# Kernel tuning notes

Measured on AMD Instinct MI355X. Metric: run time of the kernel, lower is better.

The kernel has to match this reference:

```python
import jax, jax.numpy as jnp
import numpy as np

B, L, D = 4, 2048, 1024
H, DH = 16, 64
W = 128            # window_len
CS, R = 32, 1      # chunk_size, chunk_rank
CACHE = 2048
NCC = CACHE // CS * R   # compressed cache vectors (64)
NCB = L // CS * R       # compressed block vectors (64)
NC = NCC + NCB          # total compressed vectors (128)
NQ = L // CS            # query chunks (64)
T = L // W              # query tiles (16)
NEG = jnp.float32(-1e30)


def _ln(x, g, b, eps=1e-5):
    m = x.mean(-1, keepdims=True)
    v = ((x - m) ** 2).mean(-1, keepdims=True)
    return (x - m) * jax.lax.rsqrt(v + eps) * g + b


def _scores(x, Wd, bd):
    # dconv_1 + per-chunk softmax over chunk_size positions
    b = x.shape[0]; nc = x.shape[1] // CS
    s = (x @ Wd + bd).reshape(b, nc, CS, H, R)
    s = jnp.transpose(s, (0, 3, 1, 4, 2))          # b,H,nc,R,CS
    return jax.nn.softmax(s.astype(jnp.float32), axis=-1).astype(x.dtype)


def _compress(x, sc):
    b = x.shape[0]; nc = x.shape[1] // CS
    xv = jnp.transpose(x.reshape(b, nc, CS, H, DH), (0, 3, 1, 2, 4))  # b,H,nc,CS,DH
    return (sc @ xv).reshape(b, H, nc * R, DH)


def _heads(x):
    b, l, _ = x.shape
    return jnp.transpose(x.reshape(b, l, H, DH), (0, 2, 1, 3))


def _rel_shift(x):
    # Transformer-XL style relative shift, chunk variant (zeros enter from padding)
    b = x.shape[0]; nc = x.shape[-1]
    x5 = jnp.transpose(x.reshape(b, H, NQ, CS, nc), (0, 1, 3, 2, 4))  # b,H,CS,NQ,nc
    xp = jnp.pad(x5, ((0, 0), (0, 0), (0, 0), (0, 0), (0, R))).reshape(b, H, CS, NQ * (nc + R))
    idx = NQ * R + jnp.arange(NQ)[:, None] * nc + jnp.arange(nc)[None, :]
    out = jnp.take(xp, idx.reshape(-1), axis=-1).reshape(b, H, CS, NQ, nc)
    return jnp.transpose(out, (0, 1, 3, 2, 4)).reshape(b, H, L, nc)


def _forward(h, h_cache, key_pe, pos_win, Wq, Wk, Wv, Wo, Wd, bd, Wr, br, Wrc, brc,
             r_r_bias, r_w_bias, g_dproj, b_dproj, g_win, b_win, mask):
    b = h.shape[0]
    q = _heads(h @ Wq) / np.float32(np.sqrt(DH))       # b,H,L,DH (pre-scaled)

    # --- compressed cache keys/values ---
    hcc = _compress(h_cache, _scores(h_cache, Wd, bd))           # b,H,NCC,DH
    hcm = jnp.transpose(hcc, (0, 2, 1, 3)).reshape(b, -1, D)
    k_cache = _heads(_ln(hcm @ Wk, g_dproj, b_dproj))
    v_cache = _heads(_ln(hcm @ Wv, g_dproj, b_dproj))

    # --- sliding window keys/values (last W of cache + current block) ---
    k_bp = h @ Wk
    v_bp = h @ Wv
    hw = h_cache[:, -W:]
    k_win = _ln(jnp.concatenate([hw @ Wk, k_bp], 1), g_win, b_win)   # b, W+L, D
    v_win = _ln(jnp.concatenate([hw @ Wv, v_bp], 1), g_win, b_win)

    # --- compressed current-block keys/values ---
    sc = _scores(h, Wd, bd)
    k_bpc = _heads(_ln(jnp.transpose(_compress(k_bp, sc), (0, 2, 1, 3)).reshape(b, -1, D), g_dproj, b_dproj))
    v_bpc = _heads(_ln(jnp.transpose(_compress(v_bp, sc), (0, 2, 1, 3)).reshape(b, -1, D), g_dproj, b_dproj))
    k_comp = jnp.concatenate([k_cache, k_bpc], 2)     # b,H,NC,DH
    v_comp = jnp.concatenate([v_cache, v_bpc], 2)

    # --- windowed attention (tiled, as_strided equivalent via gather) ---
    ti = jnp.arange(T)[:, None] * W + jnp.arange(2 * W)[None, :]     # (T, 2W)
    k_t = jnp.transpose(k_win[:, ti].reshape(b, T, 2 * W, H, DH), (0, 3, 1, 2, 4))  # b,H,T,2W,DH
    v_t = jnp.transpose(v_win[:, ti].reshape(b, T, 2 * W, H, DH), (0, 3, 1, 2, 4))
    q_t = q.reshape(b, H, T, W, DH)
    aw = jnp.einsum('bhtqd,bhtkd->bhtqk', q_t + r_w_bias, k_t)       # b,H,T,W,2W
    # diagonal extraction: row q keeps cols q+1 .. q+W (the W causal window keys)
    dcol = jnp.arange(W)[:, None] + 1 + jnp.arange(W)[None, :]       # (W, W)
    aw = jnp.take_along_axis(aw, dcol[None, None, None], axis=-1).reshape(b, H, L, W)
    pos_t = (pos_win @ Wr + br).reshape(W, H, DH)
    aw = aw + jnp.einsum('bhld,whd->bhlw', q + r_r_bias, pos_t)

    # --- compressed (chunk) attention ---
    ac = jnp.einsum('bhld,bhcd->bhlc', q, k_comp)
    pos_c = (key_pe @ Wrc + brc).reshape(NC, H, DH)
    ac = ac + _rel_shift(jnp.einsum('bhld,chd->bhlc', q, pos_c))
    ac = jnp.where(mask, NEG, ac.reshape(b, H, NQ, CS, NC)).reshape(b, H, L, NC)

    # --- joint softmax over [compressed | window] ---
    full = jax.nn.softmax(jnp.concatenate([ac, aw], -1).astype(jnp.float32), -1).astype(h.dtype)
    ac, aw = full[..., :NC], full[..., NC:]

    # --- put_tiles: scatter window probs back to tiled 2W layout (inverse of diag extract) ---
    awt = aw.reshape(b, H, T, W, W)
    awp = jnp.pad(awt, ((0, 0), (0, 0), (0, 0), (0, 0), (1, W)))     # last dim 1+2W, zeros outside band
    col = jnp.clip(jnp.arange(2 * W)[None, :] - jnp.arange(W)[:, None], 0, 2 * W)
    aw_t = jnp.take_along_axis(awp, col[None, None, None], axis=-1)  # b,H,T,W,2W

    out = jnp.einsum('bhlc,bhcd->bhld', ac, v_comp) + \
          jnp.einsum('bhtqk,bhtkd->bhtqd', aw_t, v_t).reshape(b, H, L, DH)
    out = jnp.transpose(out, (0, 2, 1, 3)).reshape(b, L, D)
    return out @ Wo


def setup_inputs() -> dict:
    key = jax.random.key(0)
    ks = jax.random.split(key, 16)
    p = lambda i, shape: jax.random.normal(ks[i], shape, jnp.float32) * 0.02
    inp = dict(
        h=jax.random.normal(ks[0], (B, L, D), jnp.float32),
        h_cache=jax.random.normal(ks[1], (B, CACHE, D), jnp.float32),
        key_pe=jax.random.normal(ks[2], (NC, D), jnp.float32),
        pos_embed_window=jax.random.normal(ks[3], (W, D), jnp.float32),
        Wq=p(4, (D, D)), Wk=p(5, (D, D)), Wv=p(6, (D, D)), Wo=p(7, (D, D)),
        Wd=p(8, (D, H * R)), bd=jnp.zeros((H * R,), jnp.float32),
        Wr=p(9, (D, D)), br=jnp.zeros((D,), jnp.float32),
        Wrc=p(10, (D, D)), brc=jnp.zeros((D,), jnp.float32),
        r_r_bias=p(11, (1, H, 1, DH)), r_w_bias=p(12, (1, H, 1, 1, DH)),
        g_dproj=jnp.ones((D,), jnp.float32), b_dproj=jnp.zeros((D,), jnp.float32),
        g_win=jnp.ones((D,), jnp.float32), b_win=jnp.zeros((D,), jnp.float32),
    )
    # causal mask over compressed vectors: bp chunk c visible to query chunk j only if c < j
    jq = jnp.arange(NQ)[:, None]
    cc = jnp.arange(NCB // R)[None, :]
    mbp = jnp.repeat(cc >= jq, R, axis=1)                         # (NQ, NCB)
    mask = jnp.concatenate([jnp.zeros((NQ, NCC), bool), mbp], axis=1)
    inp['chunked_attn_mask'] = mask[None, None, :, None, :]       # (1,1,NQ,1,NC)
    return inp


def reference(h, h_cache, key_pe, pos_embed_window, Wq, Wk, Wv, Wo, Wd, bd, Wr, br,
              Wrc, brc, r_r_bias, r_w_bias, g_dproj, b_dproj, g_win, b_win,
              chunked_attn_mask):
    return _forward(h, h_cache, key_pe, pos_embed_window, Wq, Wk, Wv, Wo, Wd, bd,
                    Wr, br, Wrc, brc, r_r_bias, r_w_bias, g_dproj, b_dproj,
                    g_win, b_win, chunked_attn_mask)
```

## Files before the change

### kernel.cpp

```cpp
#include <hip/hip_runtime.h>


typedef unsigned short u16;
typedef __attribute__((ext_vector_type(8))) short short8;
typedef __attribute__((ext_vector_type(4))) float f32x4;

#define NEGINF -1e30f

__device__ __forceinline__ float bf2f(u16 u) {
    union { unsigned int i; float f; } v; v.i = ((unsigned int)u) << 16; return v.f;
}
__device__ __forceinline__ u16 f2bf(float f) {
    union { float fl; unsigned int i; } v; v.fl = f;
    unsigned int x = v.i;
    return (u16)((x + 0x7fffu + ((x >> 16) & 1u)) >> 16);
}
__device__ __forceinline__ short8 ldg8(const u16* p) { return *(const short8*)p; }

__device__ __forceinline__ void async16(const u16* g, u16* l) {
    __builtin_amdgcn_global_load_lds(
        (const __attribute__((address_space(1))) unsigned int*)g,
        (__attribute__((address_space(3))) unsigned int*)l, 16, 0, 0);
}

__global__ __launch_bounds__(256) void cast_f2b(const float* __restrict__ s,
                                                u16* __restrict__ d, int n4)
{
    int i = blockIdx.x * 256 + threadIdx.x;
    if (i >= n4) return;
    float4 v = ((const float4*)s)[i];
    u16* o = d + i * 4;
    o[0] = f2bf(v.x); o[1] = f2bf(v.y); o[2] = f2bf(v.z); o[3] = f2bf(v.w);
}

__global__ __launch_bounds__(256) void cast_win(const float* __restrict__ hc,
                                                u16* __restrict__ d)
{
    int i = blockIdx.x * 256 + threadIdx.x;
    int flat = i * 4;
    int b = flat >> 17, r = (flat >> 10) & 127, c = flat & 1023;
    float4 v = *(const float4*)(hc + ((long)b * 2048 + 1920 + r) * 1024 + c);
    u16* o = d + (long)flat;
    o[0] = f2bf(v.x); o[1] = f2bf(v.y); o[2] = f2bf(v.z); o[3] = f2bf(v.w);
}

__global__ __launch_bounds__(256) void cast_transpose6(
    const float* __restrict__ W0, const float* __restrict__ W1,
    const float* __restrict__ W2, const float* __restrict__ W3,
    const float* __restrict__ W4, const float* __restrict__ W5,
    u16* __restrict__ D0, u16* __restrict__ D1, u16* __restrict__ D2,
    u16* __restrict__ D3, u16* __restrict__ D4, u16* __restrict__ D5)
{
    const int z = blockIdx.z;
    const float* W = (z == 0) ? W0 : (z == 1) ? W1 : (z == 2) ? W2
                   : (z == 3) ? W3 : (z == 4) ? W4 : W5;
    u16* WT = (z == 0) ? D0 : (z == 1) ? D1 : (z == 2) ? D2
            : (z == 3) ? D3 : (z == 4) ? D4 : D5;

    __shared__ float t[32][33];
    const int bx = blockIdx.x, by = blockIdx.y;
    const int tx = threadIdx.x & 31, ty = threadIdx.x >> 5;
    #pragma unroll
    for (int p = 0; p < 4; ++p) {
        int k = by * 32 + ty + p * 8;
        t[ty + p * 8][tx] = W[(long)k * 1024 + bx * 32 + tx];
    }
    __syncthreads();
    #pragma unroll
    for (int p = 0; p < 4; ++p) {
        int n = ty + p * 8;
        WT[((long)(bx * 32 + n)) * 1024 + by * 32 + tx] = f2bf(t[tx][n]);
    }
}

__global__ __launch_bounds__(256) void cast_wd(const float* __restrict__ Wd,
                                               u16* __restrict__ WdB)
{
    int e = blockIdx.x * 256 + threadIdx.x;
    if (e < 16384) {
        int n = e & 15, k = e >> 4;
        WdB[n * 1024 + k] = f2bf(Wd[e]);
    }
}

#define GEMM_P3_BODY(EPILOGUE)                                                  \
    const int tid = threadIdx.x;                                                \
    const int bm = blockIdx.x, bn = blockIdx.y;                                 \
    const int K = 1024, NT = 32;                                                \
    __shared__ __align__(16) u16 As[3 * 128 * 32];                              \
    __shared__ __align__(16) u16 Bs[3 * 128 * 32];                              \
    const int lane = tid & 63, wv = tid >> 6;                                   \
    const int l15 = lane & 15, quad = lane >> 4;                                \
    const int wm = (wv & 1) * 64, wn = (wv >> 1) * 64;                          \
    f32x4 acc[4][4];                                                            \
    _Pragma("unroll")                                                           \
    for (int i = 0; i < 4; ++i)                                                 \
        _Pragma("unroll")                                                       \
        for (int j = 0; j < 4; ++j) acc[i][j] = (f32x4){0.f, 0.f, 0.f, 0.f};    \
    const int srow = wv * 32 + (lane >> 2);                                     \
    const int scol = (lane & 3) * 8;                                            \
    const u16* a_src  = A  + (long)(bm * 128 + srow) * K + scol;                \
    const u16* a_src2 = a_src + (long)16 * K;                                   \
    const u16* b_src  = Bt + (long)(bn * 128 + srow) * K + scol;                \
    const u16* b_src2 = b_src + (long)16 * K;                                   \
    const int lofs0 = (wv * 32) * 32;                                           \
    const int lofs1 = (wv * 32 + 16) * 32;                                      \
    auto stage = [&](int t, int cur) {                                          \
        const int k0 = t * 32;                                                  \
        async16(a_src  + k0, &As[cur * 4096 + lofs0]);                          \
        async16(a_src2 + k0, &As[cur * 4096 + lofs1]);                          \
        async16(b_src  + k0, &Bs[cur * 4096 + lofs0]);                          \
        async16(b_src2 + k0, &Bs[cur * 4096 + lofs1]);                          \
    };                                                                          \
    stage(0, 0); stage(1, 1);                                                   \
    int cur = 0;                                                                \
    for (int t = 0; t < NT; ++t) {                                              \
        if (t == NT - 1)                                                        \
            asm volatile("s_waitcnt vmcnt(0) lgkmcnt(0)\ns_barrier" ::: "memory"); \
        else                                                                    \
            asm volatile("s_waitcnt vmcnt(4) lgkmcnt(0)\ns_barrier" ::: "memory"); \
        int nxt = cur + 2; if (nxt >= 3) nxt -= 3;                              \
        if (t + 2 < NT) stage(t + 2, nxt);                                      \
        const u16* as = &As[cur * 4096];                                        \
        const u16* bs = &Bs[cur * 4096];                                        \
        short8 af[4], bfr[4];                                                   \
        _Pragma("unroll")                                                       \
        for (int i = 0; i < 4; ++i)                                             \
            af[i] = *(const short8*)&as[(wm + i * 16 + l15) * 32 + quad * 8];   \
        _Pragma("unroll")                                                       \
        for (int j = 0; j < 4; ++j)                                             \
            bfr[j] = *(const short8*)&bs[(wn + j * 16 + l15) * 32 + quad * 8];  \
        _Pragma("unroll")                                                       \
        for (int i = 0; i < 4; ++i)                                             \
            _Pragma("unroll")                                                   \
            for (int j = 0; j < 4; ++j)                                         \
                acc[i][j] = __builtin_amdgcn_mfma_f32_16x16x32_bf16(af[i], bfr[j], acc[i][j], 0, 0, 0); \
        cur = (cur + 1 == 3) ? 0 : cur + 1;                                     \
    }                                                                           \
    EPILOGUE

__global__ __launch_bounds__(256) void gemm_qkv3(
    const u16* __restrict__ A, const u16* __restrict__ Bt,
    u16* __restrict__ q_ws, float* __restrict__ kbp, float* __restrict__ vbp)
{
    GEMM_P3_BODY({
        const int mat = bn >> 3;
        _Pragma("unroll")
        for (int i = 0; i < 4; ++i) {
            _Pragma("unroll")
            for (int j = 0; j < 4; ++j) {
                int col = (bn & 7) * 128 + wn + j * 16 + l15;
                _Pragma("unroll")
                for (int r = 0; r < 4; ++r) {
                    int row = bm * 128 + wm + i * 16 + quad * 4 + r;
                    float v = acc[i][j][r];
                    long idx = (long)row * 1024 + col;
                    if (mat == 0)      q_ws[idx] = f2bf(v * 0.125f);
                    else if (mat == 1) kbp[idx] = v;
                    else               vbp[idx] = v;
                }
            }
        }
    })
}

__global__ __launch_bounds__(256) void gemm_out3(
    const u16* __restrict__ A, const u16* __restrict__ Bt,
    float* __restrict__ Cf)
{
    GEMM_P3_BODY({
        _Pragma("unroll")
        for (int i = 0; i < 4; ++i) {
            _Pragma("unroll")
            for (int j = 0; j < 4; ++j) {
                int col = bn * 128 + wn + j * 16 + l15;
                _Pragma("unroll")
                for (int r = 0; r < 4; ++r) {
                    int row = bm * 128 + wm + i * 16 + quad * 4 + r;
                    Cf[(long)row * 1024 + col] = acc[i][j][r];
                }
            }
        }
    })
}

struct GJob {
    const u16* A; long ab;
    const u16* Bt;
    float* Cf; u16* Cb; long cb;
    const float* bias; float scale;
};

// ... 54 lines not shown
        for (int jx = 0; jx < 4; ++jx) {
            int col = bn * 128 + wn + jx * 16 + l15;
            float bsv = j.bias ? j.bias[col] : 0.f;
            #pragma unroll
            for (int r = 0; r < 4; ++r) {
                int row = bm * 128 + wm + i * 16 + quad * 4 + r;
                float v = acc[i][jx][r] * j.scale + bsv;
                long idx = coff + (long)row * N + col;
                if (j.Cf) j.Cf[idx] = v;
                if (j.Cb) j.Cb[idx] = f2bf(v);
            }
        }
    }
}

__global__ __launch_bounds__(256) void gemm_dual(GJob j0, GJob j1, int nz0, int N, int K)
{
    const bool first = ((int)blockIdx.z < nz0);
    const int bz = first ? blockIdx.z : blockIdx.z - nz0;
    if (first) gemm_core128(j0, bz, blockIdx.x, blockIdx.y, N, K);
    else       gemm_core128(j1, bz, blockIdx.x, blockIdx.y, N, K);
}

__global__ __launch_bounds__(256) void gemm_multi4(GJob j0, GJob j1, GJob j2, GJob j3,
                                                   int n0, int n1, int n2, int N, int K)
{
    const int z = blockIdx.z;
    if (z < n0)                gemm_core128(j0, z, blockIdx.x, blockIdx.y, N, K);
    else if (z < n0 + n1)      gemm_core128(j1, z - n0, blockIdx.x, blockIdx.y, N, K);
    else if (z < n0 + n1 + n2) gemm_core128(j2, z - n0 - n1, blockIdx.x, blockIdx.y, N, K);
    else                       gemm_core128(j3, z - n0 - n1 - n2, blockIdx.x, blockIdx.y, N, K);
}

__global__ __launch_bounds__(256) void scores_compress(
    const float* __restrict__ srcF, const u16* __restrict__ srcB, long src_bstride,
    const u16* __restrict__ WdB, const float* __restrict__ bd,
    u16* __restrict__ out_comp, long comp_bstride,
    float* __restrict__ out_sc, long sc_bstride)
{
    const int c = blockIdx.x, b = blockIdx.y;
    const int tid = threadIdx.x;
    const int lane = tid & 63, wv = tid >> 6;
    const int l15 = lane & 15, quad = lane >> 4;

    __shared__ __align__(16) u16 srcs[32][1032];
    __shared__ float sred[4][32][16];
    __shared__ float s_sm[32][16];

    if (srcB) {
        const u16* sb = srcB + (long)b * src_bstride + (long)c * 32 * 1024;
        for (int e = tid; e < 4096; e += 256) {
            int flat = e * 8;
            int row = flat >> 10, col = flat & 1023;
            *(short8*)&srcs[row][col] = ldg8(sb + (long)row * 1024 + col);
        }
    } else {
        const float* sb = srcF + (long)b * src_bstride + (long)c * 32 * 1024;
        for (int e = tid; e < 8192; e += 256) {
            int flat = e * 4;
            int row = flat >> 10, col = flat & 1023;
            float4 v = *(const float4*)(sb + (long)row * 1024 + col);
            u16* dp = &srcs[row][col];
            dp[0] = f2bf(v.x); dp[1] = f2bf(v.y); dp[2] = f2bf(v.z); dp[3] = f2bf(v.w);
        }
    }
    __syncthreads();

    {
        f32x4 acc0 = {0.f,0.f,0.f,0.f}, acc1 = {0.f,0.f,0.f,0.f};
        const int kq = wv * 256;
        #pragma unroll
        for (int kc = 0; kc < 8; ++kc) {
            int off = kq + kc * 32 + quad * 8;
            short8 bf_ = ldg8(WdB + (long)l15 * 1024 + off);
            short8 a0 = *(const short8*)&srcs[l15][off];
            short8 a1 = *(const short8*)&srcs[16 + l15][off];
            acc0 = __builtin_amdgcn_mfma_f32_16x16x32_bf16(a0, bf_, acc0, 0, 0, 0);
            acc1 = __builtin_amdgcn_mfma_f32_16x16x32_bf16(a1, bf_, acc1, 0, 0, 0);
        }
        #pragma unroll
        for (int r = 0; r < 4; ++r) {
            sred[wv][quad * 4 + r][l15]      = acc0[r];
            sred[wv][16 + quad * 4 + r][l15] = acc1[r];
        }
    }
    __syncthreads();
    for (int idx = tid; idx < 512; idx += 256) {
        int i = idx >> 4, hd = idx & 15;
        s_sm[i][hd] = bd[hd] + sred[0][i][hd] + sred[1][i][hd]
                            + sred[2][i][hd] + sred[3][i][hd];
    }
    __syncthreads();

    if (tid < 16) {
        int hd = tid;
        float m = NEGINF;
        for (int i = 0; i < 32; ++i) m = fmaxf(m, s_sm[i][hd]);
        float s = 0.f;
        for (int i = 0; i < 32; ++i) s += __expf(s_sm[i][hd] - m);
        float inv = 1.f / s;
        for (int i = 0; i < 32; ++i) s_sm[i][hd] = __expf(s_sm[i][hd] - m) * inv;
    }
    __syncthreads();

    if (out_sc) {
        for (int idx = tid; idx < 512; idx += 256) {
            int hd = idx >> 5, i = idx & 31;
            out_sc[(long)b * sc_bstride + ((long)hd * 64 + c) * 32 + i] = s_sm[i][hd];
        }
    }
    if (out_comp) {
        #pragma unroll
        for (int p = 0; p < 4; ++p) {
            int j = tid + p * 256;
            int hd = j >> 6;
            float acc = 0.f;
            for (int i = 0; i < 32; ++i) acc += s_sm[i][hd] * bf2f(srcs[i][j]);
            out_comp[(long)b * comp_bstride + (long)c * 1024 + j] = f2bf(acc);
        }
    }
}

__global__ __launch_bounds__(256) void compress_kv_ln(
    const float* __restrict__ kbp, const float* __restrict__ vbp,
    const float* __restrict__ sc,
    const float* __restrict__ g, const float* __restrict__ be,
    u16* __restrict__ k_comp, u16* __restrict__ vcT)
{
    const int c = blockIdx.x, b = blockIdx.y;
    const int tid = threadIdx.x;
    const int lane = tid & 63, wv = tid >> 6;

    __shared__ float scw[16][32];
    __shared__ float red[4][4];

    for (int idx = tid; idx < 512; idx += 256) {
        int hd = idx >> 5, i = idx & 31;
        scw[hd][i] = sc[((long)(b * 16 + hd) * 64 + c) * 32 + i];
    }
    __syncthreads();

    float xk[4], xv[4];
    #pragma unroll
    for (int p = 0; p < 4; ++p) {
        int j = tid + p * 256;
        int hd = j >> 6;
        float ak = 0.f, av = 0.f;
        for (int i = 0; i < 32; ++i) {
            float w = scw[hd][i];
            long off = ((long)b * 2048 + c * 32 + i) * 1024 + j;
            ak += w * kbp[off];
            av += w * vbp[off];
        }
        xk[p] = ak; xv[p] = av;
    }
    float sk = 0.f, qk = 0.f, sv = 0.f, qv = 0.f;
    #pragma unroll
    for (int p = 0; p < 4; ++p) { sk += xk[p]; qk += xk[p]*xk[p]; sv += xv[p]; qv += xv[p]*xv[p]; }
    for (int off = 32; off; off >>= 1) {
        sk += __shfl_xor(sk, off); qk += __shfl_xor(qk, off);
        sv += __shfl_xor(sv, off); qv += __shfl_xor(qv, off);
    }
    if (lane == 0) { red[0][wv] = sk; red[1][wv] = qk; red[2][wv] = sv; red[3][wv] = qv; }
    __syncthreads();
    sk = red[0][0] + red[0][1] + red[0][2] + red[0][3];
    qk = red[1][0] + red[1][1] + red[1][2] + red[1][3];
    sv = red[2][0] + red[2][1] + red[2][2] + red[2][3];
    qv = red[3][0] + red[3][1] + red[3][2] + red[3][3];
    const float inv_n = 1.f / 1024.f;
    float mk = sk * inv_n, mv = sv * inv_n;
    float ik = rsqrtf(fmaxf(qk * inv_n - mk * mk, 0.f) + 1e-5f);
    float iv = rsqrtf(fmaxf(qv * inv_n - mv * mv, 0.f) + 1e-5f);
    #pragma unroll
    for (int p = 0; p < 4; ++p) {
        int j = tid + p * 256;
        k_comp[((long)b * 128 + 64 + c) * 1024 + j] = f2bf((xk[p] - mk) * ik * g[j] + be[j]);
        vcT[((long)b * 1024 + j) * 128 + 64 + c]   = f2bf((xv[p] - mv) * iv * g[j] + be[j]);
    }
}

__global__ __launch_bounds__(256) void ln_rows_kv(
    const float* __restrict__ kc, const float* __restrict__ vc,
    const float* __restrict__ g, const float* __restrict__ be,
    u16* __restrict__ k_comp, u16* __restrict__ vcT)
{
    const int gr = blockIdx.x;
    const int b = gr >> 6, r = gr & 63;
    const float* pk = kc + ((long)b * 64 + r) * 1024;
    const float* pv = vc + ((long)b * 64 + r) * 1024;
    const int tid = threadIdx.x;
    const int lane = tid & 63, wv = tid >> 6;

    __shared__ float red[4][4];
    float xk[4], xv[4];
    float smk = 0.f, sqk = 0.f, smv = 0.f, sqv = 0.f;
    #pragma unroll
    for (int p = 0; p < 4; ++p) {
        xk[p] = pk[tid + p * 256];
        xv[p] = pv[tid + p * 256];
        smk += xk[p]; sqk += xk[p] * xk[p];
        smv += xv[p]; sqv += xv[p] * xv[p];
    }
    for (int off = 32; off; off >>= 1) {
        smk += __shfl_xor(smk, off); sqk += __shfl_xor(sqk, off);
        smv += __shfl_xor(smv, off); sqv += __shfl_xor(sqv, off);
    }
    if (lane == 0) { red[0][wv] = smk; red[1][wv] = sqk; red[2][wv] = smv; red[3][wv] = sqv; }
    __syncthreads();
    smk = red[0][0] + red[0][1] + red[0][2] + red[0][3];
    sqk = red[1][0] + red[1][1] + red[1][2] + red[1][3];
    smv = red[2][0] + red[2][1] + red[2][2] + red[2][3];
    sqv = red[3][0] + red[3][1] + red[3][2] + red[3][3];
    const float inv_n = 1.f / 1024.f;
    float mk = smk * inv_n, mv = smv * inv_n;
    float ik = rsqrtf(fmaxf(sqk * inv_n - mk * mk, 0.f) + 1e-5f);
    float iv = rsqrtf(fmaxf(sqv * inv_n - mv * mv, 0.f) + 1e-5f);
    #pragma unroll
    for (int p = 0; p < 4; ++p) {
        int j = tid + p * 256;
        k_comp[((long)b * 128 + r) * 1024 + j] = f2bf((xk[p] - mk) * ik * g[j] + be[j]);
        vcT[((long)b * 1024 + j) * 128 + r]    = f2bf((xv[p] - mv) * iv * g[j] + be[j]);
    }
}

__global__ __launch_bounds__(256) void row_stats2(
    const float* __restrict__ s1, const float* __restrict__ s2, long src_bstride,
    float2* __restrict__ d1, float2* __restrict__ d2, long dst_bstride,
    long dst_row_off, int rows_per_batch)
{
    const int gr = blockIdx.x;
    const int b = gr / rows_per_batch, r = gr % rows_per_batch;
    const float* p1 = s1 + (long)b * src_bstride + (long)r * 1024;
    const float* p2 = s2 + (long)b * src_bstride + (long)r * 1024;
    const int tid = threadIdx.x;
    const int lane = tid & 63, wv = tid >> 6;

    __shared__ float red[4][4];
    float sm1 = 0.f, sq1 = 0.f, sm2 = 0.f, sq2 = 0.f;
    #pragma unroll
    for (int p = 0; p < 4; ++p) {
        float x = p1[tid + p * 256];
        float y = p2[tid + p * 256];
        sm1 += x; sq1 += x * x;
        sm2 += y; sq2 += y * y;
    }
    for (int off = 32; off; off >>= 1) {
        sm1 += __shfl_xor(sm1, off); sq1 += __shfl_xor(sq1, off);
        sm2 += __shfl_xor(sm2, off); sq2 += __shfl_xor(sq2, off);
    }
    if (lane == 0) { red[0][wv] = sm1; red[1][wv] = sq1; red[2][wv] = sm2; red[3][wv] = sq2; }
    __syncthreads();
    if (tid == 0) {
        sm1 = red[0][0] + red[0][1] + red[0][2] + red[0][3];
        sq1 = red[1][0] + red[1][1] + red[1][2] + red[1][3];
        sm2 = red[2][0] + red[2][1] + red[2][2] + red[2][3];
        sq2 = red[3][0] + red[3][1] + red[3][2] + red[3][3];
        float m1 = sm1 * (1.f / 1024.f);
        float i1 = rsqrtf(fmaxf(sq1 * (1.f / 1024.f) - m1 * m1, 0.f) + 1e-5f);
        float m2 = sm2 * (1.f / 1024.f);
        float i2 = rsqrtf(fmaxf(sq2 * (1.f / 1024.f) - m2 * m2, 0.f) + 1e-5f);
        d1[(long)b * dst_bstride + dst_row_off + r] = make_float2(m1, i1);
        d2[(long)b * dst_bstride + dst_row_off + r] = make_float2(m2, i2);
    }
}

__global__ __launch_bounds__(256) void win_apply(
    const float* __restrict__ kcw, const float* __restrict__ vcw,
    const float* __restrict__ kbp, const float* __restrict__ vbp,
    const float2* __restrict__ st_kw, const float2* __restrict__ st_vw,
    const float* __restrict__ g_w, const float* __restrict__ b_w,
    u16* __restrict__ kwin, u16* __restrict__ vwinT)
{
    const int tt = blockIdx.x, dc = blockIdx.y, b = blockIdx.z;
    const int t0 = tt * 64, d0 = dc * 64;
    const int tid = threadIdx.x;

    __shared__ u16 vt[64][74];

    const int r = tid >> 2;
    const int dsub = (tid & 3) * 16;
    const int t = t0 + r;
    const float* ks; const float* vs;
    if (t < 128) {
        ks = kcw + ((long)b * 128 + t) * 1024;
        vs = vcw + ((long)b * 128 + t) * 1024;
    } else {
        ks = kbp + ((long)b * 2048 + t - 128) * 1024;
        vs = vbp + ((long)b * 2048 + t - 128) * 1024;
    }
    float2 sk = st_kw[(long)b * 2176 + t];
    float2 sv = st_vw[(long)b * 2176 + t];
    #pragma unroll
    for (int j = 0; j < 16; j += 4) {
        int d = d0 + dsub + j;
        float4 kv = *(const float4*)(ks + d);
        float4 vv = *(const float4*)(vs + d);
        float4 g4 = *(const float4*)(g_w + d);
        float4 b4 = *(const float4*)(b_w + d);
        u16 ko[4];
        ko[0] = f2bf((kv.x - sk.x) * sk.y * g4.x + b4.x);
        ko[1] = f2bf((kv.y - sk.x) * sk.y * g4.y + b4.y);
        ko[2] = f2bf((kv.z - sk.x) * sk.y * g4.z + b4.z);
        ko[3] = f2bf((kv.w - sk.x) * sk.y * g4.w + b4.w);
        *(uint2*)&kwin[((long)b * 2176 + t) * 1024 + d] = *(const uint2*)ko;
        vt[r][dsub + j + 0] = f2bf((vv.x - sv.x) * sv.y * g4.x + b4.x);
        vt[r][dsub + j + 1] = f2bf((vv.y - sv.x) * sv.y * g4.y + b4.y);
        vt[r][dsub + j + 2] = f2bf((vv.z - sv.x) * sv.y * g4.z + b4.z);
        vt[r][dsub + j + 3] = f2bf((vv.w - sv.x) * sv.y * g4.w + b4.w);
    }
    __syncthreads();
    #pragma unroll
    for (int pass = 0; pass < 16; ++pass) {
        int dd = (tid >> 6) + pass * 4;
        int rr = tid & 63;
        int crow = t0 + rr;
        if (crow >= 1)
            vwinT[((long)b * 1024 + d0 + dd) * 2176 + crow - 1] = vt[rr][dd];
    }
}

__global__ __launch_bounds__(256, 4) void attention(
    const u16* __restrict__ qb,
    const u16* __restrict__ kcb,
    const u16* __restrict__ vcT,
    const u16* __restrict__ kwb,
    const u16* __restrict__ vwT,
    const u16* __restrict__ pcb,
    const u16* __restrict__ ptb,
    const float* __restrict__ r_w,
// ... 103 lines not shown
                for (int j = 0; j < 8; ++j) f[j] = (short)f2bf(bf2f((u16)qv[j]) + bb[j]);
                qf[kc][hf] = f;
            }
        }
        for (int nt = wv; nt < 10; nt += 4) {
            int t = nt * 16 + l15;
            int row = l0 + 1 + t; if (row > 2175) row = 2175;
            f32x4 a0 = {0.f,0.f,0.f,0.f}, a1 = {0.f,0.f,0.f,0.f};
            #pragma unroll
            for (int kc = 0; kc < 2; ++kc) {
                int k0 = kc * 32;
                short8 bk = ldg8(kwb + ((long)(b * 2176 + row)) * 1024 + h * 64 + k0 + quad * 8);
                a0 = __builtin_amdgcn_mfma_f32_16x16x32_bf16(qf[kc][0], bk, a0, 0, 0, 0);
                a1 = __builtin_amdgcn_mfma_f32_16x16x32_bf16(qf[kc][1], bk, a1, 0, 0, 0);
            }
            s1a[nw] = a0; s1b[nw] = a1; nts[nw] = nt; ++nw;
        }
    }
    __builtin_amdgcn_s_setprio(0);
    __syncthreads();
    for (int i = 0; i < nw; ++i) {
        int t = nts[i] * 16 + l15;
        #pragma unroll
        for (int r = 0; r < 4; ++r) {
            int r0 = quad * 4 + r;
            int w0 = t - r0;
            if (w0 >= 0 && w0 < 128) L[r0 * 260 + 128 + w0] += s1a[i][r];
            int r1 = 16 + quad * 4 + r;
            int w1 = t - r1;
            if (w1 >= 0 && w1 < 128) L[r1 * 260 + 128 + w1] += s1b[i][r];
        }
    }
    __syncthreads();

    #pragma unroll
    for (int rr = 0; rr < 8; ++rr) {
        const int r = wv * 8 + rr;
        float4 v = *(const float4*)&L[r * 260 + lane * 4];
        float m = fmaxf(fmaxf(v.x, v.y), fmaxf(v.z, v.w));
        for (int off = 32; off; off >>= 1) m = fmaxf(m, __shfl_xor(m, off));
        float e0 = __expf(v.x - m), e1 = __expf(v.y - m);
        float e2 = __expf(v.z - m), e3 = __expf(v.w - m);
        float s = (e0 + e1) + (e2 + e3);
        for (int off = 32; off; off >>= 1) s += __shfl_xor(s, off);
        float inv = 1.f / s;
        e0 *= inv; e1 *= inv; e2 *= inv; e3 *= inv;
        u16* rowP = Lu + (long)r * 520;
        if (lane < 32) {
            u16 pk[4] = {f2bf(e0), f2bf(e1), f2bf(e2), f2bf(e3)};
            *(uint2*)&rowP[lane * 4] = *(const uint2*)pk;
        } else {
            const int l = lane - 32;
            const int t = 4 * l + r;
            u16* p = rowP + 160 + t;
            p[0] = f2bf(e0); p[1] = f2bf(e1); p[2] = f2bf(e2); p[3] = f2bf(e3);
            const int tz = (l < r) ? l : 128 + l;
            rowP[160 + tz] = 0;
        }
    }
    __syncthreads();

    __builtin_amdgcn_s_setprio(1);
    const int n0d = wv * 16;
    f32x4 o0 = {0.f,0.f,0.f,0.f}, o1 = {0.f,0.f,0.f,0.f};
    #pragma unroll
    for (int kc = 0; kc < 4; ++kc) {
        int k0 = kc * 32;
        short8 bv = ldg8(vcT + ((long)(b * 1024 + h * 64 + n0d + l15)) * 128 + k0 + quad * 8);
        short8 av0 = *(const short8*)(Lu + (long)l15 * 520 + k0 + quad * 8);
        short8 av1 = *(const short8*)(Lu + (long)(16 + l15) * 520 + k0 + quad * 8);
        o0 = __builtin_amdgcn_mfma_f32_16x16x32_bf16(av0, bv, o0, 0, 0, 0);
        o1 = __builtin_amdgcn_mfma_f32_16x16x32_bf16(av1, bv, o1, 0, 0, 0);
    }
    #pragma unroll
    for (int kc = 0; kc < 5; ++kc) {
        int k0 = kc * 32;
        short8 bv = ldg8(vwT + ((long)(b * 1024 + h * 64 + n0d + l15)) * 2176 + l0 + k0 + quad * 8);
        short8 av0 = *(const short8*)(Lu + (long)l15 * 520 + 160 + k0 + quad * 8);
        short8 av1 = *(const short8*)(Lu + (long)(16 + l15) * 520 + 160 + k0 + quad * 8);
        o0 = __builtin_amdgcn_mfma_f32_16x16x32_bf16(av0, bv, o0, 0, 0, 0);
        o1 = __builtin_amdgcn_mfma_f32_16x16x32_bf16(av1, bv, o1, 0, 0, 0);
    }
    __builtin_amdgcn_s_setprio(0);
    #pragma unroll
    for (int r = 0; r < 4; ++r) {
        int r0 = quad * 4 + r, r1 = 16 + quad * 4 + r;
        attn_o[((long)(b * 2048 + l0 + r0)) * 1024 + h * 64 + n0d + l15] = f2bf(o0[r]);
        attn_o[((long)(b * 2048 + l0 + r1)) * 1024 + h * 64 + n0d + l15] = f2bf(o1[r]);
    }
}

extern "C" void kernel_launch(void* const* d_in, const int* in_sizes, int n_in,
                              void* d_out, int out_size, void* d_ws, size_t ws_size,
                              hipStream_t stream)
{
    (void)in_sizes; (void)n_in; (void)out_size; (void)ws_size;

    const float* h       = (const float*)d_in[0];
    const float* h_cache = (const float*)d_in[1];
    const float* key_pe  = (const float*)d_in[2];
    const float* pos_w   = (const float*)d_in[3];
    const float* Wq      = (const float*)d_in[4];
    const float* Wk      = (const float*)d_in[5];
    const float* Wv      = (const float*)d_in[6];
    const float* Wo      = (const float*)d_in[7];
    const float* Wd      = (const float*)d_in[8];
    const float* bd      = (const float*)d_in[9];
    const float* Wr      = (const float*)d_in[10];
    const float* br      = (const float*)d_in[11];
    const float* Wrc     = (const float*)d_in[12];
    const float* brc     = (const float*)d_in[13];
    const float* r_r     = (const float*)d_in[14];
    const float* r_w     = (const float*)d_in[15];
    const float* g_d     = (const float*)d_in[16];
    const float* b_d     = (const float*)d_in[17];
    const float* g_w     = (const float*)d_in[18];
    const float* b_w     = (const float*)d_in[19];

    char* ws = (char*)d_ws;
    size_t off = 0;
    auto alloc = [&](size_t bytes) -> void* {
        void* p = ws + off; off += (bytes + 255) & ~(size_t)255; return p;
    };
    u16* hB     = (u16*)alloc((size_t)8192 * 1024 * 2);
    u16* hcwB   = (u16*)alloc((size_t)4 * 128 * 1024 * 2);
    u16* WqkvT  = (u16*)alloc((size_t)3 * 1024 * 1024 * 2);
    u16* WoT    = (u16*)alloc((size_t)1024 * 1024 * 2);
    u16* WrT    = (u16*)alloc((size_t)1024 * 1024 * 2);
    u16* WrcT   = (u16*)alloc((size_t)1024 * 1024 * 2);
    u16* pwB    = (u16*)alloc((size_t)128 * 1024 * 2);
    u16* kpeB   = (u16*)alloc((size_t)128 * 1024 * 2);
    u16* WdB    = (u16*)alloc((size_t)16 * 1024 * 2);
    u16*   q_ws   = (u16*)alloc((size_t)8192 * 1024 * 2);
    float* kbp    = (float*)alloc((size_t)8192 * 1024 * 4);
    float* vbp    = (float*)alloc((size_t)8192 * 1024 * 4);
    u16*   attn_o = (u16*)alloc((size_t)8192 * 1024 * 2);
    float* kcw    = (float*)alloc((size_t)4 * 128 * 1024 * 4);
    float* vcw    = (float*)alloc((size_t)4 * 128 * 1024 * 4);
    u16*   hcm    = (u16*)alloc((size_t)4 * 64 * 1024 * 2);
    float* kc_raw = (float*)alloc((size_t)4 * 64 * 1024 * 4);
    float* vc_raw = (float*)alloc((size_t)4 * 64 * 1024 * 4);
    float* sc_blk = (float*)alloc((size_t)4 * 16 * 64 * 32 * 4);
    u16*   k_comp = (u16*)alloc((size_t)4 * 128 * 1024 * 2);
    u16*   vcT    = (u16*)alloc((size_t)4 * 1024 * 128 * 2);
    float2* st_kw = (float2*)alloc((size_t)4 * 2176 * 8);
    float2* st_vw = (float2*)alloc((size_t)4 * 2176 * 8);
    u16*   pos_tb = (u16*)alloc((size_t)128 * 1024 * 2);
    u16*   pos_cb = (u16*)alloc((size_t)128 * 1024 * 2);
    u16*   kwin   = (u16*)alloc((size_t)4 * 2176 * 1024 * 2);
    u16*   vwinT  = (u16*)alloc((size_t)4 * 1024 * 2176 * 2 + 256);

    const u16* WkT = WqkvT + (size_t)1024 * 1024;
    const u16* WvT = WqkvT + (size_t)2 * 1024 * 1024;

    const dim3 blk(256);

    cast_f2b<<<dim3(8192), blk, 0, stream>>>(h, hB, 2097152);
    cast_win<<<dim3(512), blk, 0, stream>>>(h_cache, hcwB);
    cast_transpose6<<<dim3(32,32,6), blk, 0, stream>>>(
        Wq, Wk, Wv, Wo, Wr, Wrc,
        WqkvT, WqkvT + (size_t)1024*1024, WqkvT + (size_t)2*1024*1024,
        WoT, WrT, WrcT);
    cast_f2b<<<dim3(128), blk, 0, stream>>>(pos_w, pwB, 32768);
    cast_f2b<<<dim3(128), blk, 0, stream>>>(key_pe, kpeB, 32768);
    cast_wd<<<dim3(64), blk, 0, stream>>>(Wd, WdB);

    {
        GJob jk = { hcwB, (long)128*1024, WkT, kcw, nullptr, (long)128*1024, nullptr, 1.f };
        GJob jv = { hcwB, (long)128*1024, WvT, vcw, nullptr, (long)128*1024, nullptr, 1.f };
        GJob jt = { pwB,  0, WrT,  nullptr, pos_tb, 0, br,  1.f };
        GJob jc = { kpeB, 0, WrcT, nullptr, pos_cb, 0, brc, 1.f };
        gemm_multi4<<<dim3(1,8,10), blk, 0, stream>>>(jk, jv, jt, jc, 4, 4, 1, 1024, 1024);
    }

    gemm_qkv3<<<dim3(64,24,1), blk, 0, stream>>>(hB, WqkvT, q_ws, kbp, vbp);

    scores_compress<<<dim3(64,4), blk, 0, stream>>>(h_cache, nullptr, (long)2048*1024, WdB, bd,
                                                    hcm, (long)64*1024, nullptr, 0);
    scores_compress<<<dim3(64,4), blk, 0, stream>>>(nullptr, hB, (long)2048*1024, WdB, bd,
                                                    nullptr, 0, sc_blk, (long)16*64*32);

    {
        GJob jk = { hcm, 0, WkT, kc_raw, nullptr, 0, nullptr, 1.f };
        GJob jv = { hcm, 0, WvT, vc_raw, nullptr, 0, nullptr, 1.f };
        gemm_dual<<<dim3(2,8,2), blk, 0, stream>>>(jk, jv, 1, 1024, 1024);
    }

    compress_kv_ln<<<dim3(64,4), blk, 0, stream>>>(kbp, vbp, sc_blk, g_d, b_d, k_comp, vcT);
    ln_rows_kv<<<dim3(256), blk, 0, stream>>>(kc_raw, vc_raw, g_d, b_d, k_comp, vcT);

    row_stats2<<<dim3(512),  blk, 0, stream>>>(kcw, vcw, (long)128*1024,  st_kw, st_vw, 2176, 0,   128);
    row_stats2<<<dim3(8192), blk, 0, stream>>>(kbp, vbp, (long)2048*1024, st_kw, st_vw, 2176, 128, 2048);
    win_apply<<<dim3(34,16,4), blk, 0, stream>>>(kcw, vcw, kbp, vbp, st_kw, st_vw, g_w, b_w, kwin, vwinT);

    attention<<<dim3(64,16,4), blk, 0, stream>>>(q_ws, k_comp, vcT, kwin, vwinT,
                                                 pos_cb, pos_tb, r_w, r_r, attn_o);
    gemm_out3<<<dim3(64,8,1), blk, 0, stream>>>(attn_o, WoT, (float*)d_out);
}
```

Measured before the change: 513.9 us.

## Store block K/V projections in bf16, merge cast and stats launches, prefetch V

The block K/V projection outputs (kbp, vbp) are now written in bf16 instead of fp32, which halves their write and read traffic in the compress, row-stats and window-apply kernels. The small cast kernels, the two scores_compress launches and the two row_stats launches are each merged into a single launch to cut launch overhead. The attention kernel now loads its V fragments into registers before the softmax phase so the global loads overlap with it. The risks are rounding K/V to bf16 before the LayerNorm statistics and extra register pressure in attention.

Measured after the change: 508.5 us. About the same (-1.0%).

```diff
diff --git a/kernel.cpp b/kernel.cpp
--- a/kernel.cpp
+++ b/kernel.cpp
@@ -23,25 +23,40 @@
         (__attribute__((address_space(3))) unsigned int*)l, 16, 0, 0);
 }
 
-__global__ __launch_bounds__(256) void cast_f2b(const float* __restrict__ s,
-                                                u16* __restrict__ d, int n4)
-{
-    int i = blockIdx.x * 256 + threadIdx.x;
-    if (i >= n4) return;
-    float4 v = ((const float4*)s)[i];
-    u16* o = d + i * 4;
-    o[0] = f2bf(v.x); o[1] = f2bf(v.y); o[2] = f2bf(v.z); o[3] = f2bf(v.w);
-}
-
-__global__ __launch_bounds__(256) void cast_win(const float* __restrict__ hc,
-                                                u16* __restrict__ d)
-{
-    int i = blockIdx.x * 256 + threadIdx.x;
-    int flat = i * 4;
-    int b = flat >> 17, r = (flat >> 10) & 127, c = flat & 1023;
-    float4 v = *(const float4*)(hc + ((long)b * 2048 + 1920 + r) * 1024 + c);
-    u16* o = d + (long)flat;
-    o[0] = f2bf(v.x); o[1] = f2bf(v.y); o[2] = f2bf(v.z); o[3] = f2bf(v.w);
+__global__ __launch_bounds__(256) void cast_all(
+    const float* __restrict__ h, const float* __restrict__ hc,
+    const float* __restrict__ pos_w, const float* __restrict__ key_pe,
+    const float* __restrict__ Wd,
+    u16* __restrict__ hB, u16* __restrict__ hcwB,
+    u16* __restrict__ pwB, u16* __restrict__ kpeB, u16* __restrict__ WdB)
+{
+    const int bx = blockIdx.x, tid = threadIdx.x;
+    if (bx < 8192) {
+        int i = bx * 256 + tid;
+        float4 v = ((const float4*)h)[i];
+        u16* o = hB + (long)i * 4;
+        o[0] = f2bf(v.x); o[1] = f2bf(v.y); o[2] = f2bf(v.z); o[3] = f2bf(v.w);
+    } else if (bx < 8704) {
+        int i = (bx - 8192) * 256 + tid;
+        int flat = i * 4;
+        int b = flat >> 17, r = (flat >> 10) & 127, c = flat & 1023;
+        float4 v = *(const float4*)(hc + ((long)b * 2048 + 1920 + r) * 1024 + c);
+        u16* o = hcwB + (long)flat;
+        o[0] = f2bf(v.x); o[1] = f2bf(v.y); o[2] = f2bf(v.z); o[3] = f2bf(v.w);
+    } else if (bx < 8832) {
+        int i = (bx - 8704) * 256 + tid;
+        float4 v = ((const float4*)pos_w)[i];
+        u16* o = pwB + (long)i * 4;
+        o[0] = f2bf(v.x); o[1] = f2bf(v.y); o[2] = f2bf(v.z); o[3] = f2bf(v.w);
+    } else if (bx < 8960) {
+        int i = (bx - 8832) * 256 + tid;
+        float4 v = ((const float4*)key_pe)[i];
+        u16* o = kpeB + (long)i * 4;
+        o[0] = f2bf(v.x); o[1] = f2bf(v.y); o[2] = f2bf(v.z); o[3] = f2bf(v.w);
+    } else {
+        int e = (bx - 8960) * 256 + tid;
+        if (e < 16384) WdB[(e & 15) * 1024 + (e >> 4)] = f2bf(Wd[e]);
+    }
 }
 
 __global__ __launch_bounds__(256) void cast_transpose6(
@@ -70,16 +85,6 @@
     for (int p = 0; p < 4; ++p) {
         int n = ty + p * 8;
         WT[((long)(bx * 32 + n)) * 1024 + by * 32 + tx] = f2bf(t[tx][n]);
-    }
-}
-
-__global__ __launch_bounds__(256) void cast_wd(const float* __restrict__ Wd,
-                                               u16* __restrict__ WdB)
-{
-    int e = blockIdx.x * 256 + threadIdx.x;
-    if (e < 16384) {
-        int n = e & 15, k = e >> 4;
-        WdB[n * 1024 + k] = f2bf(Wd[e]);
     }
 }
 
@@ -141,7 +146,7 @@
 
 __global__ __launch_bounds__(256) void gemm_qkv3(
     const u16* __restrict__ A, const u16* __restrict__ Bt,
-    u16* __restrict__ q_ws, float* __restrict__ kbp, float* __restrict__ vbp)
+    u16* __restrict__ q_ws, u16* __restrict__ kbp, u16* __restrict__ vbp)
 {
     GEMM_P3_BODY({
         const int mat = bn >> 3;
@@ -156,8 +161,8 @@
                     float v = acc[i][j][r];
                     long idx = (long)row * 1024 + col;
                     if (mat == 0)      q_ws[idx] = f2bf(v * 0.125f);
-                    else if (mat == 1) kbp[idx] = v;
-                    else               vbp[idx] = v;
+                    else if (mat == 1) kbp[idx] = f2bf(v);
+                    else               vbp[idx] = f2bf(v);
                 }
             }
         }
@@ -278,13 +283,13 @@
     else                       gemm_core128(j3, z - n0 - n1 - n2, blockIdx.x, blockIdx.y, N, K);
 }
 
-__global__ __launch_bounds__(256) void scores_compress(
-    const float* __restrict__ srcF, const u16* __restrict__ srcB, long src_bstride,
+__global__ __launch_bounds__(256) void scores_compress2(
+    const float* __restrict__ hc, const u16* __restrict__ hBp,
     const u16* __restrict__ WdB, const float* __restrict__ bd,
-    u16* __restrict__ out_comp, long comp_bstride,
-    float* __restrict__ out_sc, long sc_bstride)
+    u16* __restrict__ hcm, float* __restrict__ sc_blk)
 {
     const int c = blockIdx.x, b = blockIdx.y;
+    const bool zc = (blockIdx.z == 0);
     const int tid = threadIdx.x;
     const int lane = tid & 63, wv = tid >> 6;
     const int l15 = lane & 15, quad = lane >> 4;
@@ -293,21 +298,21 @@
     __shared__ float sred[4][32][16];
     __shared__ float s_sm[32][16];
 
-    if (srcB) {
-        const u16* sb = srcB + (long)b * src_bstride + (long)c * 32 * 1024;
-        for (int e = tid; e < 4096; e += 256) {
-            int flat = e * 8;
-            int row = flat >> 10, col = flat & 1023;
-            *(short8*)&srcs[row][col] = ldg8(sb + (long)row * 1024 + col);
-        }
-    } else {
-        const float* sb = srcF + (long)b * src_bstride + (long)c * 32 * 1024;
+    if (zc) {
+        const float* sb = hc + (long)b * 2048 * 1024 + (long)c * 32 * 1024;
         for (int e = tid; e < 8192; e += 256) {
             int flat = e * 4;
             int row = flat >> 10, col = flat & 1023;
             float4 v = *(const float4*)(sb + (long)row * 1024 + col);
             u16* dp = &srcs[row][col];
             dp[0] = f2bf(v.x); dp[1] = f2bf(v.y); dp[2] = f2bf(v.z); dp[3] = f2bf(v.w);
+        }
+    } else {
+        const u16* sb = hBp + (long)b * 2048 * 1024 + (long)c * 32 * 1024;
+        for (int e = tid; e < 4096; e += 256) {
+            int flat = e * 8;
+            int row = flat >> 10, col = flat & 1023;
+            *(short8*)&srcs[row][col] = ldg8(sb + (long)row * 1024 + col);
         }
     }
     __syncthreads();
@@ -349,26 +354,25 @@
     }
     __syncthreads();
 
-    if (out_sc) {
+    if (!zc) {
         for (int idx = tid; idx < 512; idx += 256) {
             int hd = idx >> 5, i = idx & 31;
-            out_sc[(long)b * sc_bstride + ((long)hd * 64 + c) * 32 + i] = s_sm[i][hd];
-        }
-    }
-    if (out_comp) {
+            sc_blk[(long)b * (16*64*32) + ((long)hd * 64 + c) * 32 + i] = s_sm[i][hd];
+        }
+    } else {
         #pragma unroll
         for (int p = 0; p < 4; ++p) {
             int j = tid + p * 256;
             int hd = j >> 6;
             float acc = 0.f;
             for (int i = 0; i < 32; ++i) acc += s_sm[i][hd] * bf2f(srcs[i][j]);
-            out_comp[(long)b * comp_bstride + (long)c * 1024 + j] = f2bf(acc);
+            hcm[(long)b * (64*1024) + (long)c * 1024 + j] = f2bf(acc);
         }
     }
 }
 
 __global__ __launch_bounds__(256) void compress_kv_ln(
-    const float* __restrict__ kbp, const float* __restrict__ vbp,
+    const u16* __restrict__ kbp, const u16* __restrict__ vbp,
     const float* __restrict__ sc,
     const float* __restrict__ g, const float* __restrict__ be,
     u16* __restrict__ k_comp, u16* __restrict__ vcT)
@@ -386,19 +390,22 @@
     }
     __syncthreads();
 
-    float xk[4], xv[4];
-    #pragma unroll
-    for (int p = 0; p < 4; ++p) {
-        int j = tid + p * 256;
-        int hd = j >> 6;
-        float ak = 0.f, av = 0.f;
-        for (int i = 0; i < 32; ++i) {
-            float w = scw[hd][i];
-            long off = ((long)b * 2048 + c * 32 + i) * 1024 + j;
-            ak += w * kbp[off];
-            av += w * vbp[off];
-        }
-        xk[p] = ak; xv[p] = av;
+    const int j0 = tid * 4;
+    const int hd = j0 >> 6;
+    float xk[4] = {0.f,0.f,0.f,0.f}, xv[4] = {0.f,0.f,0.f,0.f};
+    const u16* kb = kbp + ((long)b * 2048 + c * 32) * 1024 + j0;
+    const u16* vb = vbp + ((long)b * 2048 + c * 32) * 1024 + j0;
+    for (int i = 0; i < 32; ++i) {
+        float w = scw[hd][i];
+        uint2 kr = *(const uint2*)(kb + (long)i * 1024);
+        uint2 vr = *(const uint2*)(vb + (long)i * 1024);
+        const u16* kp = (const u16*)&kr;
+        const u16* vp = (const u16*)&vr;
+        #pragma unroll
+        for (int p = 0; p < 4; ++p) {
+            xk[p] += w * bf2f(kp[p]);
+            xv[p] += w * bf2f(vp[p]);
+        }
     }
     float sk = 0.f, qk = 0.f, sv = 0.f, qv = 0.f;
     #pragma unroll
@@ -417,12 +424,17 @@
     float mk = sk * inv_n, mv = sv * inv_n;
     float ik = rsqrtf(fmaxf(qk * inv_n - mk * mk, 0.f) + 1e-5f);
     float iv = rsqrtf(fmaxf(qv * inv_n - mv * mv, 0.f) + 1e-5f);
-    #pragma unroll
-    for (int p = 0; p < 4; ++p) {
-        int j = tid + p * 256;
-        k_comp[((long)b * 128 + 64 + c) * 1024 + j] = f2bf((xk[p] - mk) * ik * g[j] + be[j]);
-        vcT[((long)b * 1024 + j) * 128 + 64 + c]   = f2bf((xv[p] - mv) * iv * g[j] + be[j]);
-    }
+    float4 g4 = *(const float4*)(g + j0);
+    float4 b4 = *(const float4*)(be + j0);
+    float gg[4] = {g4.x, g4.y, g4.z, g4.w};
+    float bb[4] = {b4.x, b4.y, b4.z, b4.w};
+    u16 ko[4];
+    #pragma unroll
+    for (int p = 0; p < 4; ++p) ko[p] = f2bf((xk[p] - mk) * ik * gg[p] + bb[p]);
+    *(uint2*)&k_comp[((long)b * 128 + 64 + c) * 1024 + j0] = *(const uint2*)ko;
+    #pragma unroll
+    for (int p = 0; p < 4; ++p)
+        vcT[((long)b * 1024 + j0 + p) * 128 + 64 + c] = f2bf((xv[p] - mv) * iv * gg[p] + bb[p]);
 }
 
 __global__ __launch_bounds__(256) void ln_rows_kv(
@@ -469,27 +481,49 @@
     }
 }
 
-__global__ __launch_bounds__(256) void row_stats2(
-    const float* __restrict__ s1, const float* __restrict__ s2, long src_bstride,
-    float2* __restrict__ d1, float2* __restrict__ d2, long dst_bstride,
-    long dst_row_off, int rows_per_batch)
+__global__ __launch_bounds__(256) void row_stats_all(
+    const float* __restrict__ kcw, const float* __restrict__ vcw,
+    const u16* __restrict__ kbp, const u16* __restrict__ vbp,
+    float2* __restrict__ st_k, float2* __restrict__ st_v)
 {
     const int gr = blockIdx.x;
-    const int b = gr / rows_per_batch, r = gr % rows_per_batch;
-    const float* p1 = s1 + (long)b * src_bstride + (long)r * 1024;
-    const float* p2 = s2 + (long)b * src_bstride + (long)r * 1024;
     const int tid = threadIdx.x;
     const int lane = tid & 63, wv = tid >> 6;
 
+    float sm1 = 0.f, sq1 = 0.f, sm2 = 0.f, sq2 = 0.f;
+    long dst;
+    if (gr < 512) {
+        const int b = gr >> 7, r = gr & 127;
+        const float* p1 = kcw + ((long)b * 128 + r) * 1024;
+        const float* p2 = vcw + ((long)b * 128 + r) * 1024;
+        #pragma unroll
+        for (int p = 0; p < 4; ++p) {
+            float x = p1[tid + p * 256];
+            float y = p2[tid + p * 256];
+            sm1 += x; sq1 += x * x;
+            sm2 += y; sq2 += y * y;
+        }
+        dst = (long)b * 2176 + r;
+    } else {
+        const int g2 = gr - 512;
+        const int b = g2 >> 11, r = g2 & 2047;
+        const u16* p1 = kbp + ((long)b * 2048 + r) * 1024 + tid * 4;
+        const u16* p2 = vbp + ((long)b * 2048 + r) * 1024 + tid * 4;
+        uint2 v1 = *(const uint2*)p1;
+        uint2 v2 = *(const uint2*)p2;
+        const u16* a1 = (const u16*)&v1;
+        const u16* a2 = (const u16*)&v2;
+        #pragma unroll
+        for (int p = 0; p < 4; ++p) {
+            float x = bf2f(a1[p]);
+            float y = bf2f(a2[p]);
+            sm1 += x; sq1 += x * x;
+            sm2 += y; sq2 += y * y;
+        }
+        dst = (long)b * 2176 + 128 + r;
+    }
+
     __shared__ float red[4][4];
-    float sm1 = 0.f, sq1 = 0.f, sm2 = 0.f, sq2 = 0.f;
-    #pragma unroll
-    for (int p = 0; p < 4; ++p) {
-        float x = p1[tid + p * 256];
-        float y = p2[tid + p * 256];
-        sm1 += x; sq1 += x * x;
-        sm2 += y; sq2 += y * y;
-    }
     for (int off = 32; off; off >>= 1) {
         sm1 += __shfl_xor(sm1, off); sq1 += __shfl_xor(sq1, off);
         sm2 += __shfl_xor(sm2, off); sq2 += __shfl_xor(sq2, off);
@@ -505,14 +539,14 @@
         float i1 = rsqrtf(fmaxf(sq1 * (1.f / 1024.f) - m1 * m1, 0.f) + 1e-5f);
         float m2 = sm2 * (1.f / 1024.f);
         float i2 = rsqrtf(fmaxf(sq2 * (1.f / 1024.f) - m2 * m2, 0.f) + 1e-5f);
-        d1[(long)b * dst_bstride + dst_row_off + r] = make_float2(m1, i1);
-        d2[(long)b * dst_bstride + dst_row_off + r] = make_float2(m2, i2);
+        st_k[dst] = make_float2(m1, i1);
+        st_v[dst] = make_float2(m2, i2);
     }
 }
 
 __global__ __launch_bounds__(256) void win_apply(
     const float* __restrict__ kcw, const float* __restrict__ vcw,
-    const float* __restrict__ kbp, const float* __restrict__ vbp,
+    const u16* __restrict__ kbp, const u16* __restrict__ vbp,
     const float2* __restrict__ st_kw, const float2* __restrict__ st_vw,
     const float* __restrict__ g_w, const float* __restrict__ b_w,
     u16* __restrict__ kwin, u16* __restrict__ vwinT)
@@ -526,21 +560,27 @@
     const int r = tid >> 2;
     const int dsub = (tid & 3) * 16;
     const int t = t0 + r;
-    const float* ks; const float* vs;
-    if (t < 128) {
-        ks = kcw + ((long)b * 128 + t) * 1024;
-        vs = vcw + ((long)b * 128 + t) * 1024;
-    } else {
-        ks = kbp + ((long)b * 2048 + t - 128) * 1024;
-        vs = vbp + ((long)b * 2048 + t - 128) * 1024;
-    }
     float2 sk = st_kw[(long)b * 2176 + t];
     float2 sv = st_vw[(long)b * 2176 + t];
+    const float* ksf = kcw + ((long)b * 128 + t) * 1024;
+    const float* vsf = vcw + ((long)b * 128 + t) * 1024;
+    const u16*   ksb = kbp + ((long)b * 2048 + t - 128) * 1024;
+    const u16*   vsb = vbp + ((long)b * 2048 + t - 128) * 1024;
     #pragma unroll
     for (int j = 0; j < 16; j += 4) {
         int d = d0 + dsub + j;
-        float4 kv = *(const float4*)(ks + d);
-        float4 vv = *(const float4*)(vs + d);
+        float4 kv, vv;
+        if (t < 128) {
+            kv = *(const float4*)(ksf + d);
+            vv = *(const float4*)(vsf + d);
+        } else {
+            uint2 kr = *(const uint2*)(ksb + d);
+            uint2 vr = *(const uint2*)(vsb + d);
+            const u16* kp = (const u16*)&kr;
+            const u16* vp = (const u16*)&vr;
+            kv = make_float4(bf2f(kp[0]), bf2f(kp[1]), bf2f(kp[2]), bf2f(kp[3]));
+            vv = make_float4(bf2f(vp[0]), bf2f(vp[1]), bf2f(vp[2]), bf2f(vp[3]));
+        }
         float4 g4 = *(const float4*)(g_w + d);
         float4 b4 = *(const float4*)(b_w + d);
         u16 ko[4];
@@ -710,6 +750,17 @@
         }
     }
     __syncthreads();
+
+    const int n0d = wv * 16;
+    short8 bvv[9];
+    {
+        const u16* vc = vcT + ((long)(b * 1024 + h * 64 + n0d + l15)) * 128 + quad * 8;
+        #pragma unroll
+        for (int kc = 0; kc < 4; ++kc) bvv[kc] = ldg8(vc + kc * 32);
+        const u16* vw = vwT + ((long)(b * 1024 + h * 64 + n0d + l15)) * 2176 + l0 + quad * 8;
+        #pragma unroll
+        for (int kc = 0; kc < 5; ++kc) bvv[4 + kc] = ldg8(vw + kc * 32);
+    }
 
     #pragma unroll
     for (int rr = 0; rr < 8; ++rr) {
@@ -739,25 +790,22 @@
     __syncthreads();
 
     __builtin_amdgcn_s_setprio(1);
-    const int n0d = wv * 16;
     f32x4 o0 = {0.f,0.f,0.f,0.f}, o1 = {0.f,0.f,0.f,0.f};
     #pragma unroll
     for (int kc = 0; kc < 4; ++kc) {
         int k0 = kc * 32;
-        short8 bv = ldg8(vcT + ((long)(b * 1024 + h * 64 + n0d + l15)) * 128 + k0 + quad * 8);
         short8 av0 = *(const short8*)(Lu + (long)l15 * 520 + k0 + quad * 8);
         short8 av1 = *(const short8*)(Lu + (long)(16 + l15) * 520 + k0 + quad * 8);
-        o0 = __builtin_amdgcn_mfma_f32_16x16x32_bf16(av0, bv, o0, 0, 0, 0);
-        o1 = __builtin_amdgcn_mfma_f32_16x16x32_bf16(av1, bv, o1, 0, 0, 0);
+        o0 = __builtin_amdgcn_mfma_f32_16x16x32_bf16(av0, bvv[kc], o0, 0, 0, 0);
+        o1 = __builtin_amdgcn_mfma_f32_16x16x32_bf16(av1, bvv[kc], o1, 0, 0, 0);
     }
     #pragma unroll
     for (int kc = 0; kc < 5; ++kc) {
         int k0 = kc * 32;
-        short8 bv = ldg8(vwT + ((long)(b * 1024 + h * 64 + n0d + l15)) * 2176 + l0 + k0 + quad * 8);
         short8 av0 = *(const short8*)(Lu + (long)l15 * 520 + 160 + k0 + quad * 8);
         short8 av1 = *(const short8*)(Lu + (long)(16 + l15) * 520 + 160 + k0 + quad * 8);
-        o0 = __builtin_amdgcn_mfma_f32_16x16x32_bf16(av0, bv, o0, 0, 0, 0);
-        o1 = __builtin_amdgcn_mfma_f32_16x16x32_bf16(av1, bv, o1, 0, 0, 0);
+        o0 = __builtin_amdgcn_mfma_f32_16x16x32_bf16(av0, bvv[4 + kc], o0, 0, 0, 0);
+        o1 = __builtin_amdgcn_mfma_f32_16x16x32_bf16(av1, bvv[4 + kc], o1, 0, 0, 0);
     }
     __builtin_amdgcn_s_setprio(0);
     #pragma unroll
@@ -810,8 +858,8 @@
     u16* kpeB   = (u16*)alloc((size_t)128 * 1024 * 2);
     u16* WdB    = (u16*)alloc((size_t)16 * 1024 * 2);
     u16*   q_ws   = (u16*)alloc((size_t)8192 * 1024 * 2);
-    float* kbp    = (float*)alloc((size_t)8192 * 1024 * 4);
-    float* vbp    = (float*)alloc((size_t)8192 * 1024 * 4);
+    u16*   kbp    = (u16*)alloc((size_t)8192 * 1024 * 2);
+    u16*   vbp    = (u16*)alloc((size_t)8192 * 1024 * 2);
     u16*   attn_o = (u16*)alloc((size_t)8192 * 1024 * 2);
     float* kcw    = (float*)alloc((size_t)4 * 128 * 1024 * 4);
     float* vcw    = (float*)alloc((size_t)4 * 128 * 1024 * 4);
@@ -833,15 +881,12 @@
 
     const dim3 blk(256);
 
-    cast_f2b<<<dim3(8192), blk, 0, stream>>>(h, hB, 2097152);
-    cast_win<<<dim3(512), blk, 0, stream>>>(h_cache, hcwB);
+    cast_all<<<dim3(9024), blk, 0, stream>>>(h, h_cache, pos_w, key_pe, Wd,
+                                             hB, hcwB, pwB, kpeB, WdB);
     cast_transpose6<<<dim3(32,32,6), blk, 0, stream>>>(
         Wq, Wk, Wv, Wo, Wr, Wrc,
         WqkvT, WqkvT + (size_t)1024*1024, WqkvT + (size_t)2*1024*1024,
         WoT, WrT, WrcT);
-    cast_f2b<<<dim3(128), blk, 0, stream>>>(pos_w, pwB, 32768);
-    cast_f2b<<<dim3(128), blk, 0, stream>>>(key_pe, kpeB, 32768);
-    cast_wd<<<dim3(64), blk, 0, stream>>>(Wd, WdB);
 
     {
         GJob jk = { hcwB, (long)128*1024, WkT, kcw, nullptr, (long)128*1024, nullptr, 1.f };
@@ -853,10 +898,7 @@
 
     gemm_qkv3<<<dim3(64,24,1), blk, 0, stream>>>(hB, WqkvT, q_ws, kbp, vbp);
 
-    scores_compress<<<dim3(64,4), blk, 0, stream>>>(h_cache, nullptr, (long)2048*1024, WdB, bd,
-                                                    hcm, (long)64*1024, nullptr, 0);
-    scores_compress<<<dim3(64,4), blk, 0, stream>>>(nullptr, hB, (long)2048*1024, WdB, bd,
-                                                    nullptr, 0, sc_blk, (long)16*64*32);
+    scores_compress2<<<dim3(64,4,2), blk, 0, stream>>>(h_cache, hB, WdB, bd, hcm, sc_blk);
 
     {
         GJob jk = { hcm, 0, WkT, kc_raw, nullptr, 0, nullptr, 1.f };
@@ -867,8 +909,7 @@
     compress_kv_ln<<<dim3(64,4), blk, 0, stream>>>(kbp, vbp, sc_blk, g_d, b_d, k_comp, vcT);
     ln_rows_kv<<<dim3(256), blk, 0, stream>>>(kc_raw, vc_raw, g_d, b_d, k_comp, vcT);
 
-    row_stats2<<<dim3(512),  blk, 0, stream>>>(kcw, vcw, (long)128*1024,  st_kw, st_vw, 2176, 0,   128);
-    row_stats2<<<dim3(8192), blk, 0, stream>>>(kbp, vbp, (long)2048*1024, st_kw, st_vw, 2176, 128, 2048);
+    row_stats_all<<<dim3(8704), blk, 0, stream>>>(kcw, vcw, kbp, vbp, st_kw, st_vw);
     win_apply<<<dim3(34,16,4), blk, 0, stream>>>(kcw, vcw, kbp, vbp, st_kw, st_vw, g_w, b_w, kwin, vwinT);
 
     attention<<<dim3(64,16,4), blk, 0, stream>>>(q_ws, k_comp, vcT, kwin, vwinT,
```
